# Performance work log

Hardware: AMD Instinct MI355X
Metric: run time of the kernel (lower is better)

## Reference

```python
import jax, jax.numpy as jnp
import numpy as np
from jax import lax

DIM = 128
EXP = 4
K = 7
B, D, H, W = 2, 48, 48, 48


def setup_inputs() -> dict:
    key = jax.random.key(0)
    ks = jax.random.split(key, 8)
    C, Ch = DIM, EXP * DIM
    x = jax.random.normal(ks[0], (B, C, D, H, W), dtype=jnp.float32)
    dw_w = jax.random.normal(ks[1], (C, 1, K, K, K), dtype=jnp.float32) * 0.05
    dw_b = jnp.zeros((C,), dtype=jnp.float32)
    ln_g = jnp.ones((C,), dtype=jnp.float32)
    ln_b = jnp.zeros((C,), dtype=jnp.float32)
    w1 = jax.random.normal(ks[2], (C, Ch), dtype=jnp.float32) * (1.0 / np.sqrt(C))
    b1 = jnp.zeros((Ch,), dtype=jnp.float32)
    grn_g = jnp.zeros((Ch,), dtype=jnp.float32)
    grn_b = jnp.zeros((Ch,), dtype=jnp.float32)
    w2 = jax.random.normal(ks[3], (Ch, C), dtype=jnp.float32) * (1.0 / np.sqrt(Ch))
    b2 = jnp.zeros((C,), dtype=jnp.float32)
    return {"x": x, "dw_w": dw_w, "dw_b": dw_b, "ln_g": ln_g, "ln_b": ln_b,
            "w1": w1, "b1": b1, "grn_g": grn_g, "grn_b": grn_b, "w2": w2, "b2": b2}


def reference(x, dw_w, dw_b, ln_g, ln_b, w1, b1, grn_g, grn_b, w2, b2):
    C = x.shape[1]
    pad = (K - 1) // 2
    # depthwise 3D conv, NCDHW
    y = lax.conv_general_dilated(
        x, dw_w, window_strides=(1, 1, 1),
        padding=[(pad, pad)] * 3,
        feature_group_count=C,
        dimension_numbers=("NCDHW", "OIDHW", "NCDHW"))
    y = y + dw_b[None, :, None, None, None]
    y = jnp.transpose(y, (0, 2, 3, 4, 1))  # [B,D,H,W,C] channels-last
    # LayerNorm over channels (eps=1e-6)
    mu = jnp.mean(y, axis=-1, keepdims=True)
    var = jnp.mean((y - mu) ** 2, axis=-1, keepdims=True)
    y = (y - mu) / jnp.sqrt(var + 1e-6) * ln_g + ln_b
    # pwconv1 + GELU (exact)
    h = jax.nn.gelu(jnp.einsum("bdhwc,ce->bdhwe", y, w1) + b1, approximate=False)
    # GRN: global L2 over spatial dims per channel, divisive norm over channel mean
    gx = jnp.sqrt(jnp.sum(h * h, axis=(1, 2, 3), keepdims=True))  # [B,1,1,1,Ch]
    nx = gx / (jnp.mean(gx, axis=-1, keepdims=True) + 1e-6)
    h = grn_g * (h * nx) + grn_b + h
    # pwconv2
    y = jnp.einsum("bdhwe,ec->bdhwc", h, w2) + b2
    y = jnp.transpose(y, (0, 4, 1, 2, 3))  # back to NCDHW
    return x + y
```

## Files before the change

### kernel.cpp

```cpp
#include <hip/hip_runtime.h>
#include <math.h>

#define PVOX 110592
#define CDIM 128
#define EDIM 512

typedef __attribute__((ext_vector_type(8))) short short8_t;
typedef __attribute__((ext_vector_type(4))) float float4_t;

__device__ __forceinline__ unsigned short f2bf(float f) {
  unsigned int u = __float_as_uint(f);
  unsigned int r = (u + 0x7FFFu + ((u >> 16) & 1u)) >> 16;
  return (unsigned short)r;
}
__device__ __forceinline__ float bf2f(unsigned short s) {
  return __uint_as_float(((unsigned int)s) << 16);
}
__device__ __forceinline__ int swz(int row, int col) {
  return (row << 7) + ((((col >> 3) ^ (row & 15)) << 3) | (col & 7));
}
__device__ __forceinline__ int swzO(int c, int p) {
  return (c << 7) + (p ^ ((c & 15) << 2));
}

__global__ __launch_bounds__(256) void k0_wprep(
    const float* __restrict__ w1, const float* __restrict__ w2,
    unsigned short* __restrict__ w1t, unsigned short* __restrict__ w2t) {
  int idx = blockIdx.x * 256 + threadIdx.x;
  int e = idx >> 7, c = idx & 127;
  w1t[e * 128 + c] = f2bf(w1[c * 512 + e]);
  w2t[c * 512 + e] = f2bf(w2[e * 128 + c]);
}

__global__ __launch_bounds__(256) void k1_dwconv(
    const float* __restrict__ x, const float* __restrict__ dw_w,
    const float* __restrict__ dw_b, float* __restrict__ yconv) {
  __shared__ float sx[10 * 14 * 54];
  __shared__ float sw[343];
  int bx = blockIdx.x;
  int ht = bx % 6;  int tmp = bx / 6;
  int dt = tmp % 12; tmp /= 12;
  int c = tmp & 127; int b = tmp >> 7;
  int d0 = dt * 4, h0 = ht * 8;
  const float* xp = x + (size_t)(b * 128 + c) * PVOX;
  int t = threadIdx.x;
  for (int i = t; i < 343; i += 256) sw[i] = dw_w[c * 343 + i];
  for (int i = t; i < 7560; i += 256) {
    int ww = i % 54; int r = i / 54; int hh = r % 14; int dd = r / 14;
    int gd = d0 - 3 + dd, gh = h0 - 3 + hh, gw = ww - 3;
    float v = 0.f;
    if ((unsigned)gd < 48u && (unsigned)gh < 48u && (unsigned)gw < 48u)
      v = xp[(gd * 48 + gh) * 48 + gw];
    sx[i] = v;
  }
  __syncthreads();
  int row = t >> 3;
  int chunk = t & 7;
  int td = row >> 3, th = row & 7;
  int w0 = chunk * 6;
  float bias = dw_b[c];
  float a0 = bias, a1 = bias, a2 = bias, a3 = bias, a4 = bias, a5 = bias;
  for (int kd = 0; kd < 7; kd++) {
    for (int kh = 0; kh < 7; kh++) {
      const float* rp = &sx[((td + kd) * 14 + (th + kh)) * 54 + w0];
      float v[12];
#pragma unroll
      for (int j = 0; j < 12; j++) v[j] = rp[j];
      const float* wp = &sw[(kd * 7 + kh) * 7];
#pragma unroll
      for (int kw = 0; kw < 7; kw++) {
        float wv = wp[kw];
        a0 += wv * v[kw + 0]; a1 += wv * v[kw + 1]; a2 += wv * v[kw + 2];
        a3 += wv * v[kw + 3]; a4 += wv * v[kw + 4]; a5 += wv * v[kw + 5];
      }
    }
  }
  float* op = yconv + (size_t)(b * 128 + c) * PVOX + ((d0 + td) * 48 + (h0 + th)) * 48 + w0;
  op[0] = a0; op[1] = a1; op[2] = a2; op[3] = a3; op[4] = a4; op[5] = a5;
}

__global__ __launch_bounds__(256) void k2_ln(
    const float* __restrict__ yconv, const float* __restrict__ ln_g,
    const float* __restrict__ ln_b, unsigned short* __restrict__ ycl) {
  __shared__ float sy[128 * 65];
  __shared__ float smean[64], srstd[64];
  int bx = blockIdx.x;
  int b = bx / 1728;
  int p0 = (bx % 1728) * 64;
  int t = threadIdx.x;
  int v = t & 63, c4 = t >> 6;
  const float* yp = yconv + (size_t)b * 128 * PVOX + p0;
  for (int cc = 0; cc < 32; cc++) {
    int c = cc * 4 + c4;
    sy[c * 65 + v] = yp[(size_t)c * PVOX + v];
  }
  __syncthreads();
  if (t < 64) {
    float s = 0.f, ss = 0.f;
    for (int c = 0; c < 128; c++) { float val = sy[c * 65 + t]; s += val; ss += val * val; }
    float mu = s * (1.f / 128.f);
    float var = ss * (1.f / 128.f) - mu * mu;
    smean[t] = mu; srstd[t] = rsqrtf(var + 1e-6f);
  }
  __syncthreads();
  unsigned short* op = ycl + ((size_t)b * PVOX + p0) * 128;
  for (int it = 0; it < 32; it++) {
    int idx = it * 256 + t;
    int vv = idx >> 7, c = idx & 127;
    float val = (sy[c * 65 + vv] - smean[vv]) * srstd[vv] * ln_g[c] + ln_b[c];
    op[vv * 128 + c] = f2bf(val);
  }
}

__global__ __launch_bounds__(256) void k3_pw1(
    const unsigned short* __restrict__ ycl, const unsigned short* __restrict__ w1t,
    const float* __restrict__ b1, unsigned short* __restrict__ h,
    float* __restrict__ gsum) {
  __shared__ short smem[2 * 128 * 128];
  short* sA = smem;
  short* sB = smem + 128 * 128;
  int bx = blockIdx.x;
  int et = bx & 3; int pt = bx >> 2;
  int e0 = et << 7;
  int b = (pt >= 864) ? 1 : 0;
  int t = threadIdx.x;
  for (int it = 0; it < 8; it++) {
    int flat = it * 2048 + t * 8;
    int row = flat >> 7, col = flat & 127;
    *(uint4*)&sA[swz(row, col)] = *(const uint4*)&ycl[((size_t)(pt * 128 + row)) * 128 + col];
    *(uint4*)&sB[swz(row, col)] = *(const uint4*)&w1t[(e0 + row) * 128 + col];
  }
  __syncthreads();
  int wave = t >> 6, lane = t & 63;
  int wm = (wave >> 1) * 64, wn = (wave & 1) * 64;
  int ln15 = lane & 15, q = lane >> 4;
  float4_t acc[4][4] = {};
  for (int kk = 0; kk < 4; kk++) {
    int k0 = kk * 32 + q * 8;
    short8_t af[4], bf[4];
#pragma unroll
    for (int i = 0; i < 4; i++)
      af[i] = *(const short8_t*)&sA[swz(wm + i * 16 + ln15, k0)];
#pragma unroll
    for (int j = 0; j < 4; j++)
      bf[j] = *(const short8_t*)&sB[swz(wn + j * 16 + ln15, k0)];
#pragma unroll
    for (int i = 0; i < 4; i++)
#pragma unroll
      for (int j = 0; j < 4; j++)
        acc[i][j] = __builtin_amdgcn_mfma_f32_16x16x32_bf16(af[i], bf[j], acc[i][j], 0, 0, 0);
  }
  __syncthreads();
  float biasv[4];
#pragma unroll
  for (int j = 0; j < 4; j++) biasv[j] = b1[e0 + wn + j * 16 + ln15];
  float ssq[4] = {0.f, 0.f, 0.f, 0.f};
#pragma unroll
  for (int i = 0; i < 4; i++) {
#pragma unroll
    for (int j = 0; j < 4; j++) {
      int e_local = wn + j * 16 + ln15;
#pragma unroll
      for (int r = 0; r < 4; r++) {
        float val = acc[i][j][r] + biasv[j];
        float g = 0.5f * val * (1.0f + erff(val * 0.70710678118f));
        ssq[j] += g * g;
        sA[swz(wm + i * 16 + q * 4 + r, e_local)] = (short)f2bf(g);
      }
    }
  }
#pragma unroll
  for (int j = 0; j < 4; j++) {
    ssq[j] += __shfl_xor(ssq[j], 16);
    ssq[j] += __shfl_xor(ssq[j], 32);
  }
  if (q == 0) {
#pragma unroll
    for (int j = 0; j < 4; j++)
      atomicAdd(&gsum[b * 512 + e0 + wn + j * 16 + ln15], ssq[j]);
  }
  __syncthreads();
  for (int it = 0; it < 8; it++) {
    int flat = it * 2048 + t * 8;
    int row = flat >> 7, col = flat & 127;
    *(uint4*)&h[((size_t)(pt * 128 + row)) * 512 + e0 + col] = *(const uint4*)&sA[swz(row, col)];
  }
}

__global__ __launch_bounds__(512) void k4_grn(
    const float* __restrict__ gsum, const float* __restrict__ grn_g,
    const float* __restrict__ grn_b, const float* __restrict__ w2,
    const float* __restrict__ b2, float* __restrict__ s, float* __restrict__ badd) {
  __shared__ float red[512];
  int t = threadIdx.x;
  for (int b = 0; b < 2; b++) {
    float gx = sqrtf(gsum[b * 512 + t]);
    red[t] = gx;
    __syncthreads();
    for (int off = 256; off > 0; off >>= 1) {
      if (t < off) red[t] += red[t + off];
      __syncthreads();
    }
    float mean = red[0] * (1.f / 512.f);
    __syncthreads();
    s[b * 512 + t] = 1.0f + grn_g[t] * (gx / (mean + 1e-6f));
  }
  if (t < 128) {
    float acc = b2[t];
    for (int e = 0; e < 512; e++) acc += grn_b[e] * w2[e * 128 + t];
    badd[t] = acc;
  }
}

__global__ __launch_bounds__(256) void k5_pw2(
    const unsigned short* __restrict__ h, const unsigned short* __restrict__ w2t,
    const float* __restrict__ s, const float* __restrict__ badd,
    const float* __restrict__ x, float* __restrict__ out) {
  __shared__ short smem[2 * 128 * 128];
  short* sA = smem;
  short* sB = smem + 128 * 128;
  int bx = blockIdx.x;
  int b = bx / 864;
  int p0 = (bx % 864) * 128;
  int vp0 = bx * 128;
  int t = threadIdx.x;
  int wave = t >> 6, lane = t & 63;
  int wm = (wave >> 1) * 64, wn = (wave & 1) * 64;
  int ln15 = lane & 15, q = lane >> 4;
  const float* sb = s + b * 512;
  float4_t acc[4][4] = {};
  for (int ec = 0; ec < 4; ec++) {
    int e0 = ec * 128;
    for (int it = 0; it < 8; it++) {
      int flat = it * 2048 + t * 8;
      int row = flat >> 7, col = flat & 127;
      uint4 raw = *(const uint4*)&h[((size_t)(vp0 + row)) * 512 + e0 + col];
      const unsigned short* us = (const unsigned short*)&raw;
      unsigned short ov[8];
#pragma unroll
      for (int i2 = 0; i2 < 8; i2++)
        ov[i2] = f2bf(bf2f(us[i2]) * sb[e0 + col + i2]);
      *(uint4*)&sA[swz(row, col)] = *(const uint4*)ov;
      *(uint4*)&sB[swz(row, col)] = *(const uint4*)&w2t[row * 512 + e0 + col];
    }
    __syncthreads();
    for (int kk = 0; kk < 4; kk++) {
      int k0 = kk * 32 + q * 8;
      short8_t af[4], bf[4];
#pragma unroll
      for (int i = 0; i < 4; i++)
        af[i] = *(const short8_t*)&sA[swz(wm + i * 16 + ln15, k0)];
#pragma unroll
      for (int j = 0; j < 4; j++)
        bf[j] = *(const short8_t*)&sB[swz(wn + j * 16 + ln15, k0)];
#pragma unroll
      for (int i = 0; i < 4; i++)
#pragma unroll
        for (int j = 0; j < 4; j++)
          acc[i][j] = __builtin_amdgcn_mfma_f32_16x16x32_bf16(af[i], bf[j], acc[i][j], 0, 0, 0);
    }
    __syncthreads();
  }
  float* sO = (float*)smem;
#pragma unroll
  for (int i = 0; i < 4; i++)
#pragma unroll
    for (int j = 0; j < 4; j++) {
      int c = wn + j * 16 + ln15;
#pragma unroll
      for (int r = 0; r < 4; r++)
        sO[swzO(c, wm + i * 16 + q * 4 + r)] = acc[i][j][r];
    }
  __syncthreads();
  for (int it = 0; it < 16; it++) {
    int flat4 = it * 256 + t;
    int c = flat4 >> 5, col4 = (flat4 & 31) * 4;
    float4_t v = *(const float4_t*)&sO[swzO(c, col4)];
    float bd = badd[c];
    size_t gi = (size_t)(b * 128 + c) * PVOX + p0 + col4;
    float4_t xv = *(const float4_t*)&x[gi];
    v[0] += bd + xv[0]; v[1] += bd + xv[1]; v[2] += bd + xv[2]; v[3] += bd + xv[3];
    *(float4_t*)&out[gi] = v;
  }
}

extern "C" void kernel_launch(void* const* d_in, const int* in_sizes, int n_in,
                              void* d_out, int out_size, void* d_ws, size_t ws_size,
                              hipStream_t stream) {
  (void)in_sizes; (void)n_in; (void)out_size; (void)ws_size;
  const float* x    = (const float*)d_in[0];
  const float* dw_w = (const float*)d_in[1];
  const float* dw_b = (const float*)d_in[2];
  const float* ln_g = (const float*)d_in[3];
  const float* ln_b = (const float*)d_in[4];
  const float* w1   = (const float*)d_in[5];
  const float* b1   = (const float*)d_in[6];
  const float* grn_g= (const float*)d_in[7];
  const float* grn_b= (const float*)d_in[8];
  const float* w2   = (const float*)d_in[9];
  const float* b2   = (const float*)d_in[10];
  float* outp = (float*)d_out;

  char* w = (char*)d_ws;
  float*          yconv = (float*)(w);
  unsigned short* ycl   = (unsigned short*)(w + 113246208);
  unsigned short* h     = (unsigned short*)(w + 169869312);
  float*          gsum  = (float*)(w + 396361728);
  float*          s     = (float*)(w + 396365824);
  float*          badd  = (float*)(w + 396369920);
  unsigned short* w1t   = (unsigned short*)(w + 396370432);
  unsigned short* w2t   = (unsigned short*)(w + 396501504);

  hipMemsetAsync(gsum, 0, 2 * 512 * sizeof(float), stream);
  k0_wprep<<<256, 256, 0, stream>>>(w1, w2, w1t, w2t);
  k1_dwconv<<<18432, 256, 0, stream>>>(x, dw_w, dw_b, yconv);
  k2_ln<<<3456, 256, 0, stream>>>(yconv, ln_g, ln_b, ycl);
  k3_pw1<<<6912, 256, 0, stream>>>(ycl, w1t, b1, h, gsum);
  k4_grn<<<1, 512, 0, stream>>>(gsum, grn_g, grn_b, w2, b2, s, badd);
  k5_pw2<<<1728, 256, 0, stream>>>(h, w2t, s, badd, x, outp);
}
```

Baseline: 1.166 ms.

## Retile depthwise conv with deeper depth tiles and register reuse across depth

The depthwise 7x7x7 conv now covers 16 depth slices per block instead of 4, with 384 threads. Each thread computes 8 width outputs for two adjacent depth slices, reusing every loaded shared-memory row for both outputs. Halo loads and output stores use float4 vectors, and weights are read straight from global memory instead of staged in shared memory. This cuts halo reloading and LDS traffic per output, at the cost of more registers, a larger shared tile and fewer blocks.

Measured after the change: 1.021 ms. 1.14x faster.

```diff
diff --git a/kernel.cpp b/kernel.cpp
--- a/kernel.cpp
+++ b/kernel.cpp
@@ -32,51 +32,77 @@
   w2t[c * 512 + e] = f2bf(w2[e * 128 + c]);
 }
 
-__global__ __launch_bounds__(256) void k1_dwconv(
+__global__ __launch_bounds__(384) void k1_dwconv(
     const float* __restrict__ x, const float* __restrict__ dw_w,
     const float* __restrict__ dw_b, float* __restrict__ yconv) {
-  __shared__ float sx[10 * 14 * 54];
-  __shared__ float sw[343];
+  __shared__ float sx[22 * 14 * 60];
   int bx = blockIdx.x;
   int ht = bx % 6;  int tmp = bx / 6;
-  int dt = tmp % 12; tmp /= 12;
+  int dtile = tmp % 3; tmp /= 3;
   int c = tmp & 127; int b = tmp >> 7;
-  int d0 = dt * 4, h0 = ht * 8;
+  int d0 = dtile * 16, h0 = ht * 8;
   const float* xp = x + (size_t)(b * 128 + c) * PVOX;
   int t = threadIdx.x;
-  for (int i = t; i < 343; i += 256) sw[i] = dw_w[c * 343 + i];
-  for (int i = t; i < 7560; i += 256) {
-    int ww = i % 54; int r = i / 54; int hh = r % 14; int dd = r / 14;
-    int gd = d0 - 3 + dd, gh = h0 - 3 + hh, gw = ww - 3;
-    float v = 0.f;
-    if ((unsigned)gd < 48u && (unsigned)gh < 48u && (unsigned)gw < 48u)
-      v = xp[(gd * 48 + gh) * 48 + gw];
-    sx[i] = v;
-  }
-  __syncthreads();
-  int row = t >> 3;
-  int chunk = t & 7;
-  int td = row >> 3, th = row & 7;
-  int w0 = chunk * 6;
+  for (int i = t; i < 4312; i += 384) {
+    int gi = i % 14; int rr = i / 14; int hh = rr % 14; int r = rr / 14;
+    int gd = d0 - 3 + r, gh = h0 - 3 + hh;
+    float4_t v = {0.f, 0.f, 0.f, 0.f};
+    if ((unsigned)gd < 48u && (unsigned)gh < 48u && gi >= 1 && gi <= 12)
+      v = *(const float4_t*)&xp[(gd * 48 + gh) * 48 + gi * 4 - 4];
+    *(float4_t*)&sx[r * 840 + hh * 60 + gi * 4] = v;
+  }
+  __syncthreads();
+  int wc = t % 6; int h = (t / 6) % 8; int dt = t / 48;
+  int w0 = wc * 8;
+  const float* wbase = dw_w + c * 343;
   float bias = dw_b[c];
-  float a0 = bias, a1 = bias, a2 = bias, a3 = bias, a4 = bias, a5 = bias;
-  for (int kd = 0; kd < 7; kd++) {
-    for (int kh = 0; kh < 7; kh++) {
-      const float* rp = &sx[((td + kd) * 14 + (th + kh)) * 54 + w0];
-      float v[12];
-#pragma unroll
-      for (int j = 0; j < 12; j++) v[j] = rp[j];
-      const float* wp = &sw[(kd * 7 + kh) * 7];
-#pragma unroll
-      for (int kw = 0; kw < 7; kw++) {
-        float wv = wp[kw];
-        a0 += wv * v[kw + 0]; a1 += wv * v[kw + 1]; a2 += wv * v[kw + 2];
-        a3 += wv * v[kw + 3]; a4 += wv * v[kw + 4]; a5 += wv * v[kw + 5];
+  float a0[8], a1[8];
+#pragma unroll
+  for (int i = 0; i < 8; i++) { a0[i] = bias; a1[i] = bias; }
+  for (int kh = 0; kh < 7; kh++) {
+    int hl = h + kh;
+    const float* hp = &sx[hl * 60 + w0];
+#pragma unroll
+    for (int r8 = 0; r8 < 8; r8++) {
+      int r = 2 * dt + r8;
+      const float* rp = &hp[r * 840];
+      float4_t v4[4];
+#pragma unroll
+      for (int g = 0; g < 4; g++) v4[g] = *(const float4_t*)&rp[g * 4];
+      if (r8 <= 6) {
+        const float* wr = wbase + r8 * 49 + kh * 7;
+#pragma unroll
+        for (int kw = 0; kw < 7; kw++) {
+          float wv = wr[kw];
+#pragma unroll
+          for (int wi = 0; wi < 8; wi++) {
+            int vi = wi + kw + 1;
+            a0[wi] += wv * v4[vi >> 2][vi & 3];
+          }
+        }
       }
-    }
-  }
-  float* op = yconv + (size_t)(b * 128 + c) * PVOX + ((d0 + td) * 48 + (h0 + th)) * 48 + w0;
-  op[0] = a0; op[1] = a1; op[2] = a2; op[3] = a3; op[4] = a4; op[5] = a5;
+      if (r8 >= 1) {
+        const float* wr = wbase + (r8 - 1) * 49 + kh * 7;
+#pragma unroll
+        for (int kw = 0; kw < 7; kw++) {
+          float wv = wr[kw];
+#pragma unroll
+          for (int wi = 0; wi < 8; wi++) {
+            int vi = wi + kw + 1;
+            a1[wi] += wv * v4[vi >> 2][vi & 3];
+          }
+        }
+      }
+    }
+  }
+  int dg = d0 + 2 * dt;
+  float* op0 = yconv + (size_t)(b * 128 + c) * PVOX + ((size_t)dg * 48 + (h0 + h)) * 48 + w0;
+  float* op1 = op0 + 48 * 48;
+  float4_t o;
+  o[0] = a0[0]; o[1] = a0[1]; o[2] = a0[2]; o[3] = a0[3]; *(float4_t*)&op0[0] = o;
+  o[0] = a0[4]; o[1] = a0[5]; o[2] = a0[6]; o[3] = a0[7]; *(float4_t*)&op0[4] = o;
+  o[0] = a1[0]; o[1] = a1[1]; o[2] = a1[2]; o[3] = a1[3]; *(float4_t*)&op1[0] = o;
+  o[0] = a1[4]; o[1] = a1[5]; o[2] = a1[6]; o[3] = a1[7]; *(float4_t*)&op1[4] = o;
 }
 
 __global__ __launch_bounds__(256) void k2_ln(
@@ -313,7 +339,7 @@
 
   hipMemsetAsync(gsum, 0, 2 * 512 * sizeof(float), stream);
   k0_wprep<<<256, 256, 0, stream>>>(w1, w2, w1t, w2t);
-  k1_dwconv<<<18432, 256, 0, stream>>>(x, dw_w, dw_b, yconv);
+  k1_dwconv<<<4608, 384, 0, stream>>>(x, dw_w, dw_b, yconv);
   k2_ln<<<3456, 256, 0, stream>>>(yconv, ln_g, ln_b, ycl);
   k3_pw1<<<6912, 256, 0, stream>>>(ycl, w1t, b1, h, gsum);
   k4_grn<<<1, 512, 0, stream>>>(gsum, grn_g, grn_b, w2, b2, s, badd);
```
